# Performance work log

Measured on AMD Instinct MI355X. Metric: run time of the kernel, lower is better.

The kernel has to match this reference:

```python
import jax, jax.numpy as jnp
import numpy as np

B, C, H, W = 4, 256, 56, 56
N = H * W  # 3136 tokens


def setup_inputs() -> dict:
    key = jax.random.key(0)
    ks = jax.random.split(key, 12)
    f = lambda k, s: jax.random.normal(k, s, dtype=jnp.float32)
    return {
        "feat0": f(ks[0], (B, 1, C, H, W)),
        "feat1": f(ks[1], (B, 1, C, H, W)),
        "feat2": f(ks[2], (B, 1, C, H, W)),
        "feat3": f(ks[3], (B, 1, C, H, W)),
        "hist0": jax.random.uniform(ks[4], (B, N), dtype=jnp.float32),
        "hist1": jax.random.uniform(ks[5], (B, N), dtype=jnp.float32),
        "hist2": jax.random.uniform(ks[6], (B, N), dtype=jnp.float32),
        "mask": f(ks[7], (N, N)),
        "Wv": f(ks[8], (C, C)) * 0.02,   # v_linear weight (torch layout [out,in])
        "bv": jnp.zeros((C,), jnp.float32),
        "Wl": f(ks[9], (C, 2 * C)) * 0.02,  # low_channel weight
        "bl": jnp.zeros((C,), jnp.float32),
    }


def _tokens(x5d):
    # [b,1,c,h,w] -> [b, n, c]
    b = x5d.shape[0]
    return x5d.reshape(b, C, N).transpose(0, 2, 1)


def _to5d(tok):
    # [b,n,c] -> [b,1,c,h,w]
    b = tok.shape[0]
    return tok.transpose(0, 2, 1).reshape(b, 1, C, H, W)


def reference(feat0, feat1, feat2, feat3, hist0, hist1, hist2, mask, Wv, bv, Wl, bl):
    scale = 1.0 / jnp.sqrt(jnp.float32(C))

    def stage(q_tok, feat5d):
        f = _tokens(feat5d)                                   # [b,n,c]
        corr = jnp.einsum('bnc,bmc->bnm', q_tok, f) * scale   # [b,n,n]
        p = jax.nn.softmax(corr + mask[None], axis=-1)        # masked softmax
        v = f @ Wv.T + bv                                     # v_linear
        motion = jnp.einsum('bnm,bmc->bnc', p, v)             # attention
        refined = motion + f                                  # residual
        out = jnp.concatenate([refined, f], axis=-1) @ Wl.T + bl  # low_channel
        return refined, out

    # histograms (hist0..hist2) are consumed by the original module but its
    # histogram_mask is dead code; they do not affect the math.
    q = _tokens(feat0)
    refined, out1 = stage(q, feat1)
    refined, out2 = stage(refined, feat2)
    refined, out3 = stage(refined, feat3)

    return jnp.concatenate(
        [feat0, _to5d(out1), _to5d(out2), _to5d(out3)], axis=1
    )  # [b, 4, c, h, w]
```

## Files before the change

kernel.cpp:

```cpp
#include <hip/hip_runtime.h>
#include <hip/hip_bf16.h>

#define B_   4
#define C_   256
#define N_   3136
#define QT_  196
#define NKV_ 98
#define CH_  5

typedef __attribute__((ext_vector_type(8)))  short bf16x8;
typedef __attribute__((ext_vector_type(4)))  float f32x4;
typedef __attribute__((ext_vector_type(16))) float f32x16;

#define LOG2E  1.4426950408889634f
#define SCALE2 (LOG2E / 16.0f)
#define FMAX_  20.0f

__device__ __forceinline__ unsigned short bfbits(float f) {
  __hip_bfloat16 h = __float2bfloat16(f);
  return *(unsigned short*)&h;
}
__device__ __forceinline__ unsigned cvtpk(float lo, float hi) {
  unsigned r;
  asm("v_cvt_pk_bf16_f32 %0, %1, %2" : "=v"(r) : "v"(lo), "v"(hi));
  return r;
}

__device__ __forceinline__ void gld16(const void* g, void* l) {
  __builtin_amdgcn_global_load_lds(
      (const __attribute__((address_space(1))) unsigned int*)g,
      (__attribute__((address_space(3))) unsigned int*)l, 16, 0, 0);
}

__device__ __forceinline__ int vperm(int n) {
  int k = n & 31;
  return (n & ~31) | (k & 16) | (((k >> 2) & 1) << 3) | (k & 3) | (((k >> 3) & 1) << 2);
}

__global__ __launch_bounds__(256) void transpose4_kernel(
    const float* __restrict__ f0, const float* __restrict__ f1,
    const float* __restrict__ f2, const float* __restrict__ f3,
    __hip_bfloat16* __restrict__ d0, __hip_bfloat16* __restrict__ d1,
    __hip_bfloat16* __restrict__ d2, __hip_bfloat16* __restrict__ d3,
    float* __restrict__ out) {
  __shared__ float tile[32][33];
  const int z  = blockIdx.z;
  const int fi = z >> 2;
  const int b  = z & 3;
  const float* src = (fi == 0) ? f0 : (fi == 1) ? f1 : (fi == 2) ? f2 : f3;
  __hip_bfloat16* dst = (fi == 0) ? d0 : (fi == 1) ? d1 : (fi == 2) ? d2 : d3;
  const int n0 = blockIdx.x * 32;
  const int c0 = blockIdx.y * 32;
  const int tx = threadIdx.x & 31;
  const int ty = threadIdx.x >> 5;
  const float* s = src + (size_t)b * C_ * N_;
  float* ob = out + (size_t)b * 4 * C_ * N_;
#pragma unroll
  for (int i = 0; i < 4; ++i) {
    int c = c0 + ty + i * 8;
    float v = s[(size_t)c * N_ + n0 + tx];
    tile[ty + i * 8][tx] = v;
    if (fi == 0) ob[(size_t)c * N_ + n0 + tx] = v;
  }
  __syncthreads();
  __hip_bfloat16* d = dst + (size_t)b * N_ * C_;
#pragma unroll
  for (int i = 0; i < 4; ++i) {
    int n = n0 + ty + i * 8;
    d[(size_t)n * C_ + c0 + tx] = __float2bfloat16(tile[tx][ty + i * 8]);
  }
}

__global__ __launch_bounds__(256) void cvt_all_kernel(
    const float* __restrict__ Wv, const float* __restrict__ Wl,
    const float* __restrict__ mask,
    __hip_bfloat16* __restrict__ Wvb, __hip_bfloat16* __restrict__ Wlb,
    __hip_bfloat16* __restrict__ maskb) {
  int i = blockIdx.x * 256 + threadIdx.x;
  if (i < 24576) {
    const float* src; __hip_bfloat16* dstp; int off, dst8;
    if (i < 8192) {
      off = i; src = Wv; dstp = Wvb;
      int row = off >> 5, c8 = off & 31;
      int ct = row >> 4, qt = row & 15, kk = c8 >> 2, g = c8 & 3;
      dst8 = (ct * 8 + kk) * 64 + g * 16 + qt;
    } else {
      off = i - 8192; src = Wl; dstp = Wlb;
      int row = off >> 6, c8 = off & 63;
      int ct = row >> 4, qt = row & 15, kk = c8 >> 2, g = c8 & 3;
      dst8 = (ct * 16 + kk) * 64 + g * 16 + qt;
    }
    const float4* s4 = (const float4*)src;
    float4 a = s4[2 * off], b = s4[2 * off + 1];
    union { unsigned short u[8]; bf16x8 v; } p;
    p.u[0]=bfbits(a.x); p.u[1]=bfbits(a.y); p.u[2]=bfbits(a.z); p.u[3]=bfbits(a.w);
    p.u[4]=bfbits(b.x); p.u[5]=bfbits(b.y); p.u[6]=bfbits(b.z); p.u[7]=bfbits(b.w);
    *(bf16x8*)(dstp + 8 * dst8) = p.v;
    return;
  }
  int j = i - 24576;
  if (j >= NKV_ * NKV_ * 32 * 2) return;
  const int hi  = j & 1;
  const int cl  = (j >> 1) & 31;
  const int rem = j >> 6;
  const int kt  = rem % NKV_;
  const int qu  = rem / NKV_;
  const int q   = qu * 32 + cl;
  const float* s = mask + (size_t)q * N_ + kt * 32 + 4 * hi;
  float4 a0 = *(const float4*)(s);
  float4 a1 = *(const float4*)(s + 8);
  float4 a2 = *(const float4*)(s + 16);
  float4 a3 = *(const float4*)(s + 24);
  union { unsigned short u[16]; bf16x8 v[2]; } p;
  p.u[0]=bfbits(a0.x*LOG2E); p.u[1]=bfbits(a0.y*LOG2E); p.u[2]=bfbits(a0.z*LOG2E); p.u[3]=bfbits(a0.w*LOG2E);
  p.u[4]=bfbits(a1.x*LOG2E); p.u[5]=bfbits(a1.y*LOG2E); p.u[6]=bfbits(a1.z*LOG2E); p.u[7]=bfbits(a1.w*LOG2E);
  p.u[8]=bfbits(a2.x*LOG2E); p.u[9]=bfbits(a2.y*LOG2E); p.u[10]=bfbits(a2.z*LOG2E); p.u[11]=bfbits(a2.w*LOG2E);
  p.u[12]=bfbits(a3.x*LOG2E); p.u[13]=bfbits(a3.y*LOG2E); p.u[14]=bfbits(a3.z*LOG2E); p.u[15]=bfbits(a3.w*LOG2E);
  __hip_bfloat16* d = maskb + ((size_t)rem * 32 + cl) * 32 + hi * 16;
  *(bf16x8*)(d)     = p.v[0];
  *(bf16x8*)(d + 8) = p.v[1];
}

__global__ __launch_bounds__(256) void v_linear_kernel(
    const __hip_bfloat16* __restrict__ f1, const __hip_bfloat16* __restrict__ f2,
    const __hip_bfloat16* __restrict__ f3,
    const __hip_bfloat16* __restrict__ Wv,
    const float* __restrict__ bv,
    __hip_bfloat16* __restrict__ vT0, __hip_bfloat16* __restrict__ vT1,
    __hip_bfloat16* __restrict__ vT2)
{
  const int s    = blockIdx.z;
  const int b    = blockIdx.y;
  const int nblk = blockIdx.x;
  const __hip_bfloat16* fb = (s == 0) ? f1 : (s == 1) ? f2 : f3;
  __hip_bfloat16* vT = (s == 0) ? vT0 : (s == 1) ? vT1 : vT2;
  const int wave = threadIdx.x >> 6;
  const int lane = threadIdx.x & 63;
  const int qt = lane & 15, g = lane >> 4;
  const int n0 = nblk * 64;
  const __hip_bfloat16* fbb = fb + (size_t)b * N_ * C_;
  const int c0 = wave * 64;
  f32x4 acc[4][4];
#pragma unroll
  for (int u = 0; u < 4; ++u)
#pragma unroll
    for (int j = 0; j < 4; ++j) acc[u][j] = (f32x4){0.f, 0.f, 0.f, 0.f};
#pragma unroll
  for (int kk = 0; kk < 8; ++kk) {
    int ko = kk * 32 + g * 8;
    bf16x8 bb[4];
#pragma unroll
    for (int j = 0; j < 4; ++j)
      bb[j] = *(const bf16x8*)(fbb + (size_t)(n0 + j * 16 + qt) * C_ + ko);
#pragma unroll
    for (int u = 0; u < 4; ++u) {
      bf16x8 a = *(const bf16x8*)(Wv + (size_t)(((wave * 4 + u) * 8 + kk) * 64 + lane) * 8);
#pragma unroll
      for (int j = 0; j < 4; ++j)
        acc[u][j] = __builtin_amdgcn_mfma_f32_16x16x32_bf16(a, bb[j], acc[u][j], 0, 0, 0);
    }
  }
  __hip_bfloat16* outp = vT + (size_t)b * C_ * N_;
#pragma unroll
  for (int u = 0; u < 4; ++u)
#pragma unroll
    for (int j = 0; j < 4; ++j)
#pragma unroll
      for (int r = 0; r < 4; ++r) {
        int c = c0 + u * 16 + 4 * g + r;
        int n = vperm(n0 + j * 16 + qt);
        outp[(size_t)c * N_ + n] = __float2bfloat16(acc[u][j][r] + bv[c]);
      }
}

__global__ __launch_bounds__(256, 2) void attn_kernel(
    const __hip_bfloat16* __restrict__ qb,
    const __hip_bfloat16* __restrict__ kb,
    const __hip_bfloat16* __restrict__ vT,
    const __hip_bfloat16* __restrict__ mb,
    unsigned* __restrict__ pOb,
    float* __restrict__ pML)
{
  __shared__ __hip_bfloat16 Kl[2][32 * 256];
  __shared__ __hip_bfloat16 Vl[2][32 * 256];

  const int bid   = blockIdx.x;
  const int grp   = bid % 20;
  const int qblk  = bid / 20;
  const int b     = grp / CH_;
  const int chunk = grp % CH_;
  const int wave  = threadIdx.x >> 6;
  const int lane  = threadIdx.x & 63;
  const int cl = lane & 31, hi = lane >> 5;
  const int qunit = qblk * 4 + wave;
  const bool valid = qunit < 98;
  const int qu = valid ? qunit : 97;
  const int q0row = qu * 32 + cl;
  const int t0 = (chunk * NKV_) / CH_;
  const int t1 = ((chunk + 1) * NKV_) / CH_;
  const int nt = t1 - t0;
  const int tid = threadIdx.x;

  const __hip_bfloat16* qbb = qb + (size_t)b * N_ * C_;
  const char* kbbc = (const char*)(kb + (size_t)b * N_ * C_);
  const char* vbbc = (const char*)(vT + (size_t)b * C_ * N_);
  const char* mbase = (const char*)mb + (size_t)qu * (NKV_ * 2048) + cl * 64 + hi * 32;

  bf16x8 qa[16];
#pragma unroll
  for (int ks = 0; ks < 16; ++ks)
    qa[ks] = *(const bf16x8*)(qbb + (size_t)q0row * C_ + ks * 16 + 8 * hi);

  f32x16 o[8];
#pragma unroll
  for (int ct = 0; ct < 8; ++ct)
#pragma unroll
    for (int r = 0; r < 16; ++r) o[ct][r] = 0.f;
  float lsum = 0.f;

  auto STAGE = [&](int buf, int t) {
    const char* ks0 = kbbc + (size_t)t * 32 * 512;
#pragma unroll
    for (int i = 0; i < 4; ++i) {
      int g2 = tid + i * 256;
      int ks = g2 >> 6, h2 = (g2 >> 5) & 1, key = g2 & 31;
      gld16(ks0 + key * 512 + ks * 32 + h2 * 16, (char*)&Kl[buf][0] + g2 * 16);
    }
    const char* vs0 = vbbc + (size_t)t * 64;
#pragma unroll
    for (int i = 0; i < 4; ++i) {
      int g2 = tid + i * 256;
      int st = g2 >> 9, h2 = (g2 >> 8) & 1, c = g2 & 255;
      gld16(vs0 + (size_t)c * (N_ * 2) + st * 32 + h2 * 16, (char*)&Vl[buf][0] + g2 * 16);
    }
  };

  union { uint4 v[2]; unsigned w[8]; } mm;
  auto MLOAD = [&](int t) {
    mm.v[0] = *(const uint4*)(mbase + (size_t)t * 2048);
    mm.v[1] = *(const uint4*)(mbase + (size_t)t * 2048 + 16);
  };

  STAGE(0, t0);
  MLOAD(t0);

  const int kread = hi * 512 + cl * 16;
  const int vread = hi * 4096 + cl * 16;

  for (int tt = 0; tt < nt; ++tt) {
    const int buf = tt & 1;
    const bool nl = (tt + 1 < nt);
    if (nl) STAGE(buf ^ 1, t0 + tt + 1);
    if (nl) asm volatile("s_waitcnt vmcnt(10)" ::: "memory");
    else    asm volatile("s_waitcnt vmcnt(2)"  ::: "memory");
    __builtin_amdgcn_s_barrier();

    f32x16 s;
#pragma unroll
    for (int r = 0; r < 16; ++r) s[r] = 0.f;
    if (valid) {
      const char* Kb = (const char*)&Kl[buf][0] + kread;
      __builtin_amdgcn_s_setprio(1);
#pragma unroll
      for (int ks = 0; ks < 16; ++ks) {
        bf16x8 kf = *(const bf16x8*)(Kb + ks * 1024);
        s = __builtin_amdgcn_mfma_f32_32x32x16_bf16(kf, qa[ks], s, 0, 0, 0);
      }
      __builtin_amdgcn_s_setprio(0);
    }

    if (valid) {
      float p[16];
#pragma unroll
      for (int j = 0; j < 16; ++j) {
        unsigned wo = mm.w[j >> 1];
        float mf = __uint_as_float((j & 1) ? (wo & 0xffff0000u) : (wo << 16));
        p[j] = exp2f(fmaf(s[j], SCALE2, mf) - FMAX_);
      }
      lsum += ((p[0]+p[1])+(p[2]+p[3])) + ((p[4]+p[5])+(p[6]+p[7]))
            + ((p[8]+p[9])+(p[10]+p[11])) + ((p[12]+p[13])+(p[14]+p[15]));

      union { unsigned u[4]; bf16x8 v8; } A0, A1;
#pragma unroll
      for (int k = 0; k < 4; ++k) A0.u[k] = cvtpk(p[2 * k], p[2 * k + 1]);
#pragma unroll
      for (int k = 0; k < 4; ++k) A1.u[k] = cvtpk(p[8 + 2 * k], p[9 + 2 * k]);

      const char* Vb = (const char*)&Vl[buf][0] + vread;
      __builtin_amdgcn_s_setprio(1);
#pragma unroll
      for (int ct = 0; ct < 8; ++ct) {
        bf16x8 vf0 = *(const bf16x8*)(Vb + ct * 512);
        o[ct] = __builtin_amdgcn_mfma_f32_32x32x16_bf16(A0.v8, vf0, o[ct], 0, 0, 0);
        bf16x8 vf1 = *(const bf16x8*)(Vb + 8192 + ct * 512);
        o[ct] = __builtin_amdgcn_mfma_f32_32x32x16_bf16(A1.v8, vf1, o[ct], 0, 0, 0);
      }
      __builtin_amdgcn_s_setprio(0);
    }
    if (nl) MLOAD(t0 + tt + 1);
    __builtin_amdgcn_s_barrier();
  }

  if (valid) {
    float lt = lsum + __shfl_xor(lsum, 32);
#pragma unroll
    for (int r = 0; r < 16; ++r) {
      int q = (r & 3) + 8 * (r >> 2) + 4 * hi;
      int qt16 = qu * 2 + (q >> 4);
      int row = q & 15;
      size_t ob = ((((size_t)b * QT_ + qt16) * CH_ + chunk) * 2048) + row * 128 + cl;
#pragma unroll
      for (int pp = 0; pp < 4; ++pp)
        pOb[ob + pp * 32] = cvtpk(o[2 * pp][r], o[2 * pp + 1][r]);
    }
    if (lane < 32) {
      int qt16 = qu * 2 + (cl >> 4);
      int row = cl & 15;
      float* pml = pML + (((size_t)b * QT_ + qt16) * CH_ + chunk) * 32;
      pml[row] = FMAX_;
      pml[16 + row] = lt;
    }
  }
}

__global__ __launch_bounds__(256) void combine_kernel(
    const unsigned* __restrict__ pOb, const float* __restrict__ pML,
    const __hip_bfloat16* __restrict__ fb,
    __hip_bfloat16* __restrict__ ref)
{
  __shared__ float sml[CH_ * 32];
  const int b = blockIdx.y;
  const int qtile = blockIdx.x;
  const int tid = threadIdx.x;
  const float* pml = pML + ((size_t)b * QT_ + qtile) * (CH_ * 32);
  if (tid < CH_ * 32) sml[tid] = pml[tid];
  __syncthreads();

  const int w  = tid & 127;
  const int r0 = (tid >> 7) * 8;
  const int ch_lo = 64 * (w >> 5) + (w & 31);
  const int ch_hi = ch_lo + 32;

  float wgt[CH_][8];
#pragma unroll
  for (int r = 0; r < 8; ++r) {
    int row = r0 + r;
    float M = sml[row];
#pragma unroll
    for (int ch = 1; ch < CH_; ++ch) M = fmaxf(M, sml[ch * 32 + row]);
    float L = 0.f;
#pragma unroll
    for (int ch = 0; ch < CH_; ++ch) {
      float wv = exp2f(sml[ch * 32 + row] - M);
      wgt[ch][r] = wv;
      L += wv * sml[ch * 32 + 16 + row];
    }
    float iL = 1.f / L;
#pragma unroll
    for (int ch = 0; ch < CH_; ++ch) wgt[ch][r] *= iL;
  }

  float acc_lo[8], acc_hi[8];
#pragma unroll
  for (int r = 0; r < 8; ++r) { acc_lo[r] = 0.f; acc_hi[r] = 0.f; }
  const unsigned* base = pOb + ((size_t)b * QT_ + qtile) * (CH_ * 2048) + r0 * 128 + w;
#pragma unroll
  for (int ch = 0; ch < CH_; ++ch) {
    const unsigned* p = base + ch * 2048;
#pragma unroll
    for (int r = 0; r < 8; ++r) {
      unsigned u = p[r * 128];
      acc_lo[r] += wgt[ch][r] * __uint_as_float(u << 16);
      acc_hi[r] += wgt[ch][r] * __uint_as_float(u & 0xffff0000u);
    }
  }

  const __hip_bfloat16* f = fb + ((size_t)b * N_ + qtile * 16 + r0) * C_;
  __hip_bfloat16* rf = ref + ((size_t)b * N_ + qtile * 16 + r0) * C_;
#pragma unroll
  for (int r = 0; r < 8; ++r) {
    rf[r * C_ + ch_lo] = __float2bfloat16(acc_lo[r] + __bfloat162float(f[r * C_ + ch_lo]));
    rf[r * C_ + ch_hi] = __float2bfloat16(acc_hi[r] + __bfloat162float(f[r * C_ + ch_hi]));
  }
}

__global__ __launch_bounds__(256) void out_linear_kernel(
    const __hip_bfloat16* __restrict__ refb,
    const __hip_bfloat16* __restrict__ fb,
    const __hip_bfloat16* __restrict__ Wl,
    const float* __restrict__ bl,
    float* __restrict__ out)
{
  const int b    = blockIdx.z;
  const int cblk = blockIdx.y;
  const int nblk = blockIdx.x;
  const int wave = threadIdx.x >> 6;
  const int lane = threadIdx.x & 63;
  const int qt = lane & 15, g = lane >> 4;
  const int c0 = cblk * 128 + wave * 32;
  const int n0 = nblk * 32;
  const __hip_bfloat16* rb  = refb + (size_t)b * N_ * C_;
  const __hip_bfloat16* fbb = fb  + (size_t)b * N_ * C_;
  f32x4 acc[2][2];
#pragma unroll
  for (int u = 0; u < 2; ++u)
#pragma unroll
    for (int j = 0; j < 2; ++j) acc[u][j] = (f32x4){0.f, 0.f, 0.f, 0.f};
#pragma unroll
  for (int kk = 0; kk < 16; ++kk) {
    int ko2 = (kk * 32 + g * 8) & 255;
    const __hip_bfloat16* src = (kk < 8) ? rb : fbb;
    bf16x8 bb0 = *(const bf16x8*)(src + (size_t)(n0 + qt) * C_ + ko2);
    bf16x8 bb1 = *(const bf16x8*)(src + (size_t)(n0 + 16 + qt) * C_ + ko2);
#pragma unroll
    for (int u = 0; u < 2; ++u) {
      int ct = cblk * 8 + wave * 2 + u;
      bf16x8 a = *(const bf16x8*)(Wl + (size_t)((ct * 16 + kk) * 64 + lane) * 8);
      acc[u][0] = __builtin_amdgcn_mfma_f32_16x16x32_bf16(a, bb0, acc[u][0], 0, 0, 0);
      acc[u][1] = __builtin_amdgcn_mfma_f32_16x16x32_bf16(a, bb1, acc[u][1], 0, 0, 0);
    }
  }
  float* ob = out + (size_t)b * 4 * C_ * N_;
#pragma unroll
  for (int u = 0; u < 2; ++u)
#pragma unroll
    for (int j = 0; j < 2; ++j)
#pragma unroll
      for (int r = 0; r < 4; ++r) {
        int c = c0 + u * 16 + 4 * g + r;
        int n = n0 + j * 16 + qt;
        ob[(size_t)c * N_ + n] = acc[u][j][r] + bl[c];
      }
}

extern "C" void kernel_launch(void* const* d_in, const int* in_sizes, int n_in,
                              void* d_out, int out_size, void* d_ws, size_t ws_size,
                              hipStream_t stream) {
  (void)in_sizes; (void)n_in; (void)out_size; (void)ws_size;
  const float* feat0 = (const float*)d_in[0];
  const float* feat1 = (const float*)d_in[1];
  const float* feat2 = (const float*)d_in[2];
  const float* feat3 = (const float*)d_in[3];
  const float* mask  = (const float*)d_in[7];
  const float* Wv    = (const float*)d_in[8];
  const float* bv    = (const float*)d_in[9];
  const float* Wl    = (const float*)d_in[10];
  const float* bl    = (const float*)d_in[11];
  float* out = (float*)d_out;

  const size_t TOKB = (size_t)B_ * N_ * C_ * 2;
  char* w = (char*)d_ws;
  __hip_bfloat16* q0   = (__hip_bfloat16*)(w);
  __hip_bfloat16* f1   = (__hip_bfloat16*)(w + TOKB);
  __hip_bfloat16* f2   = (__hip_bfloat16*)(w + 2 * TOKB);
  __hip_bfloat16* f3   = (__hip_bfloat16*)(w + 3 * TOKB);
  __hip_bfloat16* vT0  = (__hip_bfloat16*)(w + 4 * TOKB);
  __hip_bfloat16* vT1  = (__hip_bfloat16*)(w + 5 * TOKB);
  __hip_bfloat16* vT2  = (__hip_bfloat16*)(w + 6 * TOKB);
  char* w2 = w + 7 * TOKB;
  __hip_bfloat16* Wv_bf = (__hip_bfloat16*)(w2);
  __hip_bfloat16* Wl_bf = (__hip_bfloat16*)(w2 + 131072);
  __hip_bfloat16* maskb = (__hip_bfloat16*)(w2 + 393216);
  unsigned* pOb         = (unsigned*)(w2 + 393216 + 19668992);
  float* pML            = (float*)(w2 + 393216 + 19668992 + (size_t)B_ * QT_ * CH_ * 4096 * 2);

  dim3 tb(256);
  transpose4_kernel<<<dim3(98, 8, 16), tb, 0, stream>>>(feat0, feat1, feat2, feat3,
                                                        q0, f1, f2, f3, out);
  cvt_all_kernel<<<dim3((24576 + NKV_ * NKV_ * 64 + 255) / 256), tb, 0, stream>>>(
      Wv, Wl, mask, Wv_bf, Wl_bf, maskb);
  v_linear_kernel<<<dim3(49, 4, 3), tb, 0, stream>>>(f1, f2, f3, Wv_bf, bv,
                                                     vT0, vT1, vT2);

  const __hip_bfloat16* fs[3] = {f1, f2, f3};
  const __hip_bfloat16* vTs[3] = {vT0, vT1, vT2};
  __hip_bfloat16* refs[3] = {vT0, vT1, vT0};
  const __hip_bfloat16* q = q0;
  for (int s = 0; s < 3; ++s) {
    attn_kernel<<<dim3(500), tb, 0, stream>>>(q, fs[s], vTs[s], maskb, pOb, pML);
    combine_kernel<<<dim3(196, 4), tb, 0, stream>>>(pOb, pML, fs[s], refs[s]);
    out_linear_kernel<<<dim3(98, 2, 4), tb, 0, stream>>>(refs[s], fs[s], Wl_bf, bl,
                                                         out + (size_t)(s + 1) * C_ * N_);
    q = refs[s];
  }
}
```

Baseline: 329.3 us.

## Co-schedule previous stage's output linear with next stage's attention in one launch

Merges each stage's out_linear work into the following stage's attention launch as extra blocks (blocks past 500 run the output projection on the previous refined tokens). This cuts two kernel launches and lets the small projection GEMM fill idle CUs alongside the 500 attention blocks, instead of running serially. The merged kernel inherits attention's launch bounds and shared-memory footprint, which may constrain occupancy for the projection blocks.

```diff
diff --git a/kernel.cpp b/kernel.cpp
--- a/kernel.cpp
+++ b/kernel.cpp
@@ -173,18 +173,15 @@
       }
 }
 
-__global__ __launch_bounds__(256, 2) void attn_kernel(
-    const __hip_bfloat16* __restrict__ qb,
-    const __hip_bfloat16* __restrict__ kb,
-    const __hip_bfloat16* __restrict__ vT,
-    const __hip_bfloat16* __restrict__ mb,
-    unsigned* __restrict__ pOb,
-    float* __restrict__ pML)
+__device__ __forceinline__ void attn_body(
+    int bid,
+    const __hip_bfloat16* __restrict__ qb, const __hip_bfloat16* __restrict__ kb,
+    const __hip_bfloat16* __restrict__ vT, const __hip_bfloat16* __restrict__ mb,
+    unsigned* __restrict__ pOb, float* __restrict__ pML)
 {
   __shared__ __hip_bfloat16 Kl[2][32 * 256];
   __shared__ __hip_bfloat16 Vl[2][32 * 256];
 
-  const int bid   = blockIdx.x;
   const int grp   = bid % 20;
   const int qblk  = bid / 20;
   const int b     = grp / CH_;
@@ -323,77 +320,16 @@
   }
 }
 
-__global__ __launch_bounds__(256) void combine_kernel(
-    const unsigned* __restrict__ pOb, const float* __restrict__ pML,
-    const __hip_bfloat16* __restrict__ fb,
-    __hip_bfloat16* __restrict__ ref)
-{
-  __shared__ float sml[CH_ * 32];
-  const int b = blockIdx.y;
-  const int qtile = blockIdx.x;
-  const int tid = threadIdx.x;
-  const float* pml = pML + ((size_t)b * QT_ + qtile) * (CH_ * 32);
-  if (tid < CH_ * 32) sml[tid] = pml[tid];
-  __syncthreads();
-
-  const int w  = tid & 127;
-  const int r0 = (tid >> 7) * 8;
-  const int ch_lo = 64 * (w >> 5) + (w & 31);
-  const int ch_hi = ch_lo + 32;
-
-  float wgt[CH_][8];
-#pragma unroll
-  for (int r = 0; r < 8; ++r) {
-    int row = r0 + r;
-    float M = sml[row];
-#pragma unroll
-    for (int ch = 1; ch < CH_; ++ch) M = fmaxf(M, sml[ch * 32 + row]);
-    float L = 0.f;
-#pragma unroll
-    for (int ch = 0; ch < CH_; ++ch) {
-      float wv = exp2f(sml[ch * 32 + row] - M);
-      wgt[ch][r] = wv;
-      L += wv * sml[ch * 32 + 16 + row];
-    }
-    float iL = 1.f / L;
-#pragma unroll
-    for (int ch = 0; ch < CH_; ++ch) wgt[ch][r] *= iL;
-  }
-
-  float acc_lo[8], acc_hi[8];
-#pragma unroll
-  for (int r = 0; r < 8; ++r) { acc_lo[r] = 0.f; acc_hi[r] = 0.f; }
-  const unsigned* base = pOb + ((size_t)b * QT_ + qtile) * (CH_ * 2048) + r0 * 128 + w;
-#pragma unroll
-  for (int ch = 0; ch < CH_; ++ch) {
-    const unsigned* p = base + ch * 2048;
-#pragma unroll
-    for (int r = 0; r < 8; ++r) {
-      unsigned u = p[r * 128];
-      acc_lo[r] += wgt[ch][r] * __uint_as_float(u << 16);
-      acc_hi[r] += wgt[ch][r] * __uint_as_float(u & 0xffff0000u);
-    }
-  }
-
-  const __hip_bfloat16* f = fb + ((size_t)b * N_ + qtile * 16 + r0) * C_;
-  __hip_bfloat16* rf = ref + ((size_t)b * N_ + qtile * 16 + r0) * C_;
-#pragma unroll
-  for (int r = 0; r < 8; ++r) {
-    rf[r * C_ + ch_lo] = __float2bfloat16(acc_lo[r] + __bfloat162float(f[r * C_ + ch_lo]));
-    rf[r * C_ + ch_hi] = __float2bfloat16(acc_hi[r] + __bfloat162float(f[r * C_ + ch_hi]));
-  }
-}
-
-__global__ __launch_bounds__(256) void out_linear_kernel(
-    const __hip_bfloat16* __restrict__ refb,
-    const __hip_bfloat16* __restrict__ fb,
-    const __hip_bfloat16* __restrict__ Wl,
-    const float* __restrict__ bl,
+__device__ __forceinline__ void out_linear_body(
+    int bid,
+    const __hip_bfloat16* __restrict__ refb, const __hip_bfloat16* __restrict__ fb,
+    const __hip_bfloat16* __restrict__ Wl, const float* __restrict__ bl,
     float* __restrict__ out)
 {
-  const int b    = blockIdx.z;
-  const int cblk = blockIdx.y;
-  const int nblk = blockIdx.x;
+  const int b    = bid / 196;
+  const int rest = bid % 196;
+  const int cblk = rest / 98;
+  const int nblk = rest % 98;
   const int wave = threadIdx.x >> 6;
   const int lane = threadIdx.x & 63;
   const int qt = lane & 15, g = lane >> 4;
@@ -431,6 +367,99 @@
         int n = n0 + j * 16 + qt;
         ob[(size_t)c * N_ + n] = acc[u][j][r] + bl[c];
       }
+}
+
+__global__ __launch_bounds__(256, 2) void attn_kernel(
+    const __hip_bfloat16* __restrict__ qb, const __hip_bfloat16* __restrict__ kb,
+    const __hip_bfloat16* __restrict__ vT, const __hip_bfloat16* __restrict__ mb,
+    unsigned* __restrict__ pOb, float* __restrict__ pML)
+{
+  attn_body(blockIdx.x, qb, kb, vT, mb, pOb, pML);
+}
+
+__global__ __launch_bounds__(256, 2) void attn_out_kernel(
+    const __hip_bfloat16* __restrict__ qb, const __hip_bfloat16* __restrict__ kb,
+    const __hip_bfloat16* __restrict__ vT, const __hip_bfloat16* __restrict__ mb,
+    unsigned* __restrict__ pOb, float* __restrict__ pML,
+    const __hip_bfloat16* __restrict__ refb, const __hip_bfloat16* __restrict__ fprev,
+    const __hip_bfloat16* __restrict__ Wl, const float* __restrict__ bl,
+    float* __restrict__ outp)
+{
+  if (blockIdx.x < 500)
+    attn_body(blockIdx.x, qb, kb, vT, mb, pOb, pML);
+  else
+    out_linear_body(blockIdx.x - 500, refb, fprev, Wl, bl, outp);
+}
+
+__global__ __launch_bounds__(256) void out_linear_kernel(
+    const __hip_bfloat16* __restrict__ refb,
+    const __hip_bfloat16* __restrict__ fb,
+    const __hip_bfloat16* __restrict__ Wl,
+    const float* __restrict__ bl,
+    float* __restrict__ out)
+{
+  out_linear_body(blockIdx.x, refb, fb, Wl, bl, out);
+}
+
+__global__ __launch_bounds__(256) void combine_kernel(
+    const unsigned* __restrict__ pOb, const float* __restrict__ pML,
+    const __hip_bfloat16* __restrict__ fb,
+    __hip_bfloat16* __restrict__ ref)
+{
+  __shared__ float sml[CH_ * 32];
+  const int b = blockIdx.y;
+  const int qtile = blockIdx.x;
+  const int tid = threadIdx.x;
+  const float* pml = pML + ((size_t)b * QT_ + qtile) * (CH_ * 32);
+  if (tid < CH_ * 32) sml[tid] = pml[tid];
+  __syncthreads();
+
+  const int w  = tid & 127;
+  const int r0 = (tid >> 7) * 8;
+  const int ch_lo = 64 * (w >> 5) + (w & 31);
+  const int ch_hi = ch_lo + 32;
+
+  float wgt[CH_][8];
+#pragma unroll
+  for (int r = 0; r < 8; ++r) {
+    int row = r0 + r;
+    float M = sml[row];
+#pragma unroll
+    for (int ch = 1; ch < CH_; ++ch) M = fmaxf(M, sml[ch * 32 + row]);
+    float L = 0.f;
+#pragma unroll
+    for (int ch = 0; ch < CH_; ++ch) {
+      float wv = exp2f(sml[ch * 32 + row] - M);
+      wgt[ch][r] = wv;
+      L += wv * sml[ch * 32 + 16 + row];
+    }
+    float iL = 1.f / L;
+#pragma unroll
+    for (int ch = 0; ch < CH_; ++ch) wgt[ch][r] *= iL;
+  }
+
+  float acc_lo[8], acc_hi[8];
+#pragma unroll
+  for (int r = 0; r < 8; ++r) { acc_lo[r] = 0.f; acc_hi[r] = 0.f; }
+  const unsigned* base = pOb + ((size_t)b * QT_ + qtile) * (CH_ * 2048) + r0 * 128 + w;
+#pragma unroll
+  for (int ch = 0; ch < CH_; ++ch) {
+    const unsigned* p = base + ch * 2048;
+#pragma unroll
+    for (int r = 0; r < 8; ++r) {
+      unsigned u = p[r * 128];
+      acc_lo[r] += wgt[ch][r] * __uint_as_float(u << 16);
+      acc_hi[r] += wgt[ch][r] * __uint_as_float(u & 0xffff0000u);
+    }
+  }
+
+  const __hip_bfloat16* f = fb + ((size_t)b * N_ + qtile * 16 + r0) * C_;
+  __hip_bfloat16* rf = ref + ((size_t)b * N_ + qtile * 16 + r0) * C_;
+#pragma unroll
+  for (int r = 0; r < 8; ++r) {
+    rf[r * C_ + ch_lo] = __float2bfloat16(acc_lo[r] + __bfloat162float(f[r * C_ + ch_lo]));
+    rf[r * C_ + ch_hi] = __float2bfloat16(acc_hi[r] + __bfloat162float(f[r * C_ + ch_hi]));
+  }
 }
 
 extern "C" void kernel_launch(void* const* d_in, const int* in_sizes, int n_in,
@@ -472,15 +501,16 @@
   v_linear_kernel<<<dim3(49, 4, 3), tb, 0, stream>>>(f1, f2, f3, Wv_bf, bv,
                                                      vT0, vT1, vT2);
 
-  const __hip_bfloat16* fs[3] = {f1, f2, f3};
-  const __hip_bfloat16* vTs[3] = {vT0, vT1, vT2};
-  __hip_bfloat16* refs[3] = {vT0, vT1, vT0};
-  const __hip_bfloat16* q = q0;
-  for (int s = 0; s < 3; ++s) {
-    attn_kernel<<<dim3(500), tb, 0, stream>>>(q, fs[s], vTs[s], maskb, pOb, pML);
-    combine_kernel<<<dim3(196, 4), tb, 0, stream>>>(pOb, pML, fs[s], refs[s]);
-    out_linear_kernel<<<dim3(98, 2, 4), tb, 0, stream>>>(refs[s], fs[s], Wl_bf, bl,
-                                                         out + (size_t)(s + 1) * C_ * N_);
-    q = refs[s];
-  }
-}
+  attn_kernel<<<dim3(500), tb, 0, stream>>>(q0, f1, vT0, maskb, pOb, pML);
+  combine_kernel<<<dim3(196, 4), tb, 0, stream>>>(pOb, pML, f1, vT0);
+  attn_out_kernel<<<dim3(1284), tb, 0, stream>>>(vT0, f2, vT1, maskb, pOb, pML,
+                                                 vT0, f1, Wl_bf, bl,
+                                                 out + (size_t)1 * C_ * N_);
+  combine_kernel<<<dim3(196, 4), tb, 0, stream>>>(pOb, pML, f2, vT1);
+  attn_out_kernel<<<dim3(1284), tb, 0, stream>>>(vT1, f3, vT2, maskb, pOb, pML,
+                                                 vT1, f2, Wl_bf, bl,
+                                                 out + (size_t)2 * C_ * N_);
+  combine_kernel<<<dim3(196, 4), tb, 0, stream>>>(pOb, pML, f3, vT0);
+  out_linear_kernel<<<dim3(784), tb, 0, stream>>>(vT0, f3, Wl_bf, bl,
+                                                  out + (size_t)3 * C_ * N_);
+}
```

Measured after the change: 318.4 us. 1.03x faster.
